# Kernel optimization log

Measured on AMD Instinct MI355X. Metric: run time of the kernel, lower is better.

Reference implementation:

```python
import jax, jax.numpy as jnp
import numpy as np

HEAD_SIZE = 64
N_EMBD = 768

def setup_inputs() -> dict:
    key = jax.random.key(0)
    kx, kq, kk, kv = jax.random.split(key, 4)
    x = jax.random.normal(kx, (4, 4096, N_EMBD), dtype=jnp.float32)
    s = 1.0 / np.sqrt(N_EMBD)
    Wq = jax.random.normal(kq, (N_EMBD, HEAD_SIZE), dtype=jnp.float32) * s
    Wk = jax.random.normal(kk, (N_EMBD, HEAD_SIZE), dtype=jnp.float32) * s
    Wv = jax.random.normal(kv, (N_EMBD, HEAD_SIZE), dtype=jnp.float32) * s
    return {"x": x, "Wq": Wq, "Wk": Wk, "Wv": Wv}

def reference(x, Wq, Wk, Wv):
    b, t, c = x.shape
    h = Wq.shape[1]
    q = jnp.einsum('btc,ch->bth', x, Wq)
    k = jnp.einsum('btc,ch->bth', x, Wk)
    v = jnp.einsum('btc,ch->bth', x, Wv)
    scores = jnp.einsum('bqh,bkh->bqk', q, k) / jnp.sqrt(jnp.float32(h))
    causal = jnp.tril(jnp.ones((t, t), dtype=bool))  # [t,t]
    scores = jnp.where(causal, scores, -jnp.inf)
    attn = jax.nn.softmax(scores, axis=-1)
    return jnp.einsum('bqk,bkh->bqh', attn, v)
```

## Files before the change

kernel.cpp:

```cpp
#include <hip/hip_runtime.h>
#include <math.h>

#define BB 4
#define TT 4096
#define CC 768
#define HH 64
#define NN 192
#define LDP 72
#define GR 32
#define XSTR 776
#define SC2 0.180336880f

typedef __bf16 bf16x8 __attribute__((ext_vector_type(8)));
typedef float floatx4 __attribute__((ext_vector_type(4)));
typedef float floatx16 __attribute__((ext_vector_type(16)));
typedef unsigned short u16x8 __attribute__((ext_vector_type(8)));

__device__ inline unsigned short f2bf(float f) {
    union { __bf16 b; unsigned short u; } v;
    v.b = (__bf16)f;
    return v.u;
}
__device__ inline float bf2f(unsigned short u) {
    union { unsigned int u; float f; } v;
    v.u = (unsigned int)u << 16;
    return v.f;
}
__device__ inline unsigned cvtpk(float lo, float hi) {
    unsigned d;
    asm("v_cvt_pk_bf16_f32 %0, %1, %2" : "=v"(d) : "v"(lo), "v"(hi));
    return d;
}

__global__ __launch_bounds__(256) void wprep(const float* __restrict__ Wq,
                                             const float* __restrict__ Wk,
                                             const float* __restrict__ Wv,
                                             unsigned short* __restrict__ wtf) {
    const int idx = blockIdx.x * 256 + threadIdx.x;
    if (idx >= NN * CC) return;
    const int j = idx & 7;
    const int lane = (idx >> 3) & 63;
    const int rest = idx >> 9;
    const int kg = rest % 24;
    const int n_tile = rest / 24;
    const int c = kg * 32 + (lane >> 4) * 8 + j;
    const int n = n_tile * 16 + (lane & 15);
    const float* W = (n < 64) ? Wq : (n < 128) ? Wk : Wv;
    wtf[idx] = f2bf(W[c * HH + (n & 63)]);
}

__global__ __launch_bounds__(256) void qkv_gemm(const float* __restrict__ x,
                                                const unsigned short* __restrict__ wtf,
                                                unsigned short* __restrict__ qb,
                                                unsigned short* __restrict__ kb,
                                                unsigned short* __restrict__ vbt) {
    __shared__ unsigned short As[GR * XSTR];

    const int tid = threadIdx.x;
    const int w = tid >> 6, lane = tid & 63;
    const int l15 = lane & 15, quad = lane >> 4;
    const int m0 = blockIdx.x * GR;
    const int n0 = w * 48;
    const int nt0 = w * 3;

    const float* xbase = x + (size_t)m0 * CC;
#pragma unroll
    for (int e = 0; e < 12; ++e) {
        const int c = tid + 256 * e;
        const int r = c / 96, off = (c - r * 96) * 8;
        const float4 v0 = *(const float4*)(xbase + (size_t)c * 8);
        const float4 v1 = *(const float4*)(xbase + (size_t)c * 8 + 4);
        u16x8 pk;
        pk[0] = f2bf(v0.x); pk[1] = f2bf(v0.y); pk[2] = f2bf(v0.z); pk[3] = f2bf(v0.w);
        pk[4] = f2bf(v1.x); pk[5] = f2bf(v1.y); pk[6] = f2bf(v1.z); pk[7] = f2bf(v1.w);
        *(u16x8*)(As + r * XSTR + off) = pk;
    }
    __syncthreads();

    floatx4 acc[2][3] = {};
#pragma unroll 4
    for (int step = 0; step < 12; ++step) {
        bf16x8 a0[2], a1[2];
#pragma unroll
        for (int rg = 0; rg < 2; ++rg) {
            const unsigned short* ap = As + (16 * rg + l15) * XSTR + step * 64 + quad * 8;
            a0[rg] = *(const bf16x8*)(ap);
            a1[rg] = *(const bf16x8*)(ap + 32);
        }
#pragma unroll
        for (int j = 0; j < 3; ++j) {
            const unsigned short* bp =
                wtf + ((size_t)((nt0 + j) * 24 + 2 * step) * 64 + lane) * 8;
            const bf16x8 b0 = *(const bf16x8*)(bp);
            const bf16x8 b1 = *(const bf16x8*)(bp + 512);
#pragma unroll
            for (int rg = 0; rg < 2; ++rg) {
                acc[rg][j] = __builtin_amdgcn_mfma_f32_16x16x32_bf16(a0[rg], b0, acc[rg][j], 0, 0, 0);
                acc[rg][j] = __builtin_amdgcn_mfma_f32_16x16x32_bf16(a1[rg], b1, acc[rg][j], 0, 0, 0);
            }
        }
    }

    const int b = m0 >> 12;
#pragma unroll
    for (int j = 0; j < 3; ++j) {
        const int n = n0 + j * 16 + l15;
        const int mid = n >> 6;
        const int h = n & 63;
#pragma unroll
        for (int rg = 0; rg < 2; ++rg) {
            const int tloc = (m0 & (TT - 1)) + 16 * rg + quad * 4;
            if (mid == 2) {
                ushort4 pk;
                pk.x = f2bf(acc[rg][j][0]); pk.y = f2bf(acc[rg][j][1]);
                pk.z = f2bf(acc[rg][j][2]); pk.w = f2bf(acc[rg][j][3]);
                *(ushort4*)(vbt + ((size_t)b * HH + h) * TT + tloc) = pk;
            } else {
                unsigned short* dst = (mid == 0) ? qb : kb;
#pragma unroll
                for (int r = 0; r < 4; ++r)
                    dst[(size_t)(m0 + 16 * rg + quad * 4 + r) * HH + h] = f2bf(acc[rg][j][r]);
            }
        }
    }
}

template<int CH>
__global__ __launch_bounds__(256) void attn_part(const unsigned short* __restrict__ qb,
                                                 const unsigned short* __restrict__ kb,
                                                 const unsigned short* __restrict__ vbt,
                                                 unsigned short* __restrict__ Opart,
                                                 float* __restrict__ lsum,
                                                 float* __restrict__ out) {
    __shared__ __align__(16) unsigned short Ks[64 * 64];
    __shared__ __align__(16) unsigned short VTs[64 * 64];

    constexpr int W  = CH / 2;
    constexpr int NB = 32 / W;
    constexpr int NG = NB;
    constexpr int TOTB = W * NB * (NB + 1) / 2;

    const int b = blockIdx.x & 3;
    int rem = TOTB - 1 - (blockIdx.x >> 2);
    int g = 0;
    while (rem >= W * (g + 1)) { rem -= W * (g + 1); ++g; }
    const int qt = g * W + rem / (g + 1);
    const int ch = rem - (rem / (g + 1)) * (g + 1);

    const int q0  = qt * 128;
    const int tid = threadIdx.x;
    const int w = tid >> 6, lane = tid & 63;
    const int l31 = lane & 31, hi = lane >> 5;
    const int qbase = q0 + 32 * w;

    const unsigned short* Qb  = qb  + (size_t)b * TT * HH;
    const unsigned short* Kb  = kb  + (size_t)b * TT * HH;
    const unsigned short* VTb = vbt + (size_t)b * HH * TT;

    bf16x8 qf[4];
    {
        const unsigned short* qp = Qb + (size_t)(qbase + l31) * HH + 8 * hi;
#pragma unroll
        for (int s = 0; s < 4; ++s) qf[s] = *(const bf16x8*)(qp + 16 * s);
    }

    floatx16 o0 = {}, o1 = {};
    float lacc = 0.f;

    const int nkt = 2 * qt + 2;
    const int kt0 = ch * CH;
    const int kt1 = min(kt0 + CH, nkt);

    const int sr = tid >> 3;
    const int slot = tid & 7;
    const int swz = ((slot ^ (sr & 7)) << 3);

    const int krow_off0 = l31 * 64;
    const int ksw = (l31 & 7);
    const int vd0 = l31, vd1 = 32 + l31;

    u16x8 nk0, nk1, nv0, nv1;
    {
        const unsigned short* Kt = Kb + (size_t)(kt0 * 64) * HH;
        const unsigned short* Vt = VTb + kt0 * 64;
        nk0 = *(const u16x8*)(Kt + (size_t)sr * HH + slot * 8);
        nk1 = *(const u16x8*)(Kt + (size_t)(sr + 32) * HH + slot * 8);
        nv0 = *(const u16x8*)(Vt + (size_t)sr * TT + slot * 8);
        nv1 = *(const u16x8*)(Vt + (size_t)(sr + 32) * TT + slot * 8);
    }

    for (int kt = kt0; kt < kt1; ++kt) {
        __syncthreads();
        *(u16x8*)(Ks  + sr * 64 + swz)        = nk0;
        *(u16x8*)(Ks  + (sr + 32) * 64 + swz) = nk1;
        *(u16x8*)(VTs + sr * 64 + swz)        = nv0;
        *(u16x8*)(VTs + (sr + 32) * 64 + swz) = nv1;
        __syncthreads();

        if (kt + 1 < kt1) {
            const unsigned short* Kt = Kb + (size_t)((kt + 1) * 64) * HH;
            const unsigned short* Vt = VTb + (kt + 1) * 64;
            nk0 = *(const u16x8*)(Kt + (size_t)sr * HH + slot * 8);
            nk1 = *(const u16x8*)(Kt + (size_t)(sr + 32) * HH + slot * 8);
            nv0 = *(const u16x8*)(Vt + (size_t)sr * TT + slot * 8);
            nv1 = *(const u16x8*)(Vt + (size_t)(sr + 32) * TT + slot * 8);
        }

#pragma unroll
        for (int ks = 0; ks < 2; ++ks) {
            const int kb32 = kt * 64 + 32 * ks;
            if (kb32 > qbase + 31) continue;

            bf16x8 kc[4];
#pragma unroll
            for (int s = 0; s < 4; ++s) {
                const int sl = 2 * s + hi;
                kc[s] = *(const bf16x8*)(Ks + 32 * 64 * ks + krow_off0 + ((sl ^ ksw) << 3));
            }

            floatx16 sa = {};
#pragma unroll
            for (int s = 0; s < 4; ++s)
                sa = __builtin_amdgcn_mfma_f32_32x32x16_bf16(kc[s], qf[s], sa, 0, 0, 0);

            float st[16];
#pragma unroll
            for (int r = 0; r < 16; ++r) st[r] = sa[r] * SC2;

            if (kb32 == qbase) {
#pragma unroll
                for (int r = 0; r < 16; ++r) {
                    const int key = (r & 3) + 8 * (r >> 2) + 4 * hi;
                    if (key > l31) st[r] = -INFINITY;
                }
            }

#pragma unroll
            for (int r = 0; r < 16; ++r) {
                const float p = exp2f(st[r]);
                st[r] = p;
                lacc += p;
            }

            bf16x8 pf[2];
#pragma unroll
            for (int m = 0; m < 2; ++m) {
                const unsigned d0 = cvtpk(st[8 * m + 0], st[8 * m + 1]);
                const unsigned d1 = cvtpk(st[8 * m + 2], st[8 * m + 3]);
                const unsigned d2 = cvtpk(st[8 * m + 4], st[8 * m + 5]);
                const unsigned d3 = cvtpk(st[8 * m + 6], st[8 * m + 7]);
                const unsigned e0 = (unsigned)__shfl_xor((int)d0, 32);
                const unsigned e1 = (unsigned)__shfl_xor((int)d1, 32);
                const unsigned e2 = (unsigned)__shfl_xor((int)d2, 32);
                const unsigned e3 = (unsigned)__shfl_xor((int)d3, 32);
                union { unsigned u[4]; bf16x8 v; } pk;
                pk.u[0] = hi ? e2 : d0;
                pk.u[1] = hi ? e3 : d1;
                pk.u[2] = hi ? d2 : e0;
                pk.u[3] = hi ? d3 : e1;
                pf[m] = pk.v;
            }

            bf16x8 vv[4];
#pragma unroll
            for (int i = 0; i < 4; ++i) {
                const int db = i >> 1, m = i & 1;
                const int d = db ? vd1 : vd0;
                const int sl = 4 * ks + 2 * m + hi;
                vv[i] = *(const bf16x8*)(VTs + d * 64 + ((sl ^ (d & 7)) << 3));
            }

            o0 = __builtin_amdgcn_mfma_f32_32x32x16_bf16(vv[0], pf[0], o0, 0, 0, 0);
            o0 = __builtin_amdgcn_mfma_f32_32x32x16_bf16(vv[1], pf[1], o0, 0, 0, 0);
            o1 = __builtin_amdgcn_mfma_f32_32x32x16_bf16(vv[2], pf[0], o1, 0, 0, 0);
            o1 = __builtin_amdgcn_mfma_f32_32x32x16_bf16(vv[3], pf[1], o1, 0, 0, 0);
        }
    }

    const float l = lacc + __shfl_xor(lacc, 32);

    if (qt < W) {
        float* outp = out + ((size_t)b * TT + qbase + l31) * HH;
        const float inv = 1.f / l;
#pragma unroll
        for (int r = 0; r < 16; ++r) {
            const int dd = (r & 3) + 8 * (r >> 2) + 4 * hi;
            outp[dd]      = o0[r] * inv;
            outp[32 + dd] = o1[r] * inv;
        }
        return;
    }

    const int pbase = ((b * 32 + qt) * NG + ch) * 128;
    unsigned short* Op = Opart + ((size_t)pbase + 32 * w + l31) * HH;
#pragma unroll
    for (int a = 0; a < 4; ++a) {
        *(unsigned*)(Op + 8 * a + 4 * hi)          = cvtpk(o0[4 * a + 0], o0[4 * a + 1]);
        *(unsigned*)(Op + 8 * a + 4 * hi + 2)      = cvtpk(o0[4 * a + 2], o0[4 * a + 3]);
        *(unsigned*)(Op + 32 + 8 * a + 4 * hi)     = cvtpk(o1[4 * a + 0], o1[4 * a + 1]);
        *(unsigned*)(Op + 32 + 8 * a + 4 * hi + 2) = cvtpk(o1[4 * a + 2], o1[4 * a + 3]);
    }
    if (hi == 0) lsum[pbase + 32 * w + l31] = l;
}

template<int CH>
__global__ __launch_bounds__(256) void attn_merge(const unsigned short* __restrict__ Opart,
                                                  const float* __restrict__ lsum,
                                                  float* __restrict__ out) {
    constexpr int W  = CH / 2;
    constexpr int NG = 32 / W;
    const int g = blockIdx.x * 256 + threadIdx.x;
    const int row = g >> 3, oct = g & 7;
    const int b = row >> 12, t = row & (TT - 1);
    const int qt = t >> 7, rloc = t & 127;
    if (qt < W) return;
    const int nchunk = qt / W + 1;
    const int pbase = ((b * 32 + qt) * NG) * 128 + rloc;
    const int d0 = oct * 8;

    float L = 0.f;
    float a[8] = {};
    for (int c = 0; c < nchunk; ++c) {
        const int idx = pbase + c * 128;
        L += lsum[idx];
        const u16x8 pv = *(const u16x8*)(Opart + (size_t)idx * HH + d0);
#pragma unroll
        for (int k = 0; k < 8; ++k) a[k] += bf2f(pv[k]);
    }
    const float inv = 1.f / L;
    float4 o0, o1;
    o0.x = a[0] * inv; o0.y = a[1] * inv; o0.z = a[2] * inv; o0.w = a[3] * inv;
    o1.x = a[4] * inv; o1.y = a[5] * inv; o1.z = a[6] * inv; o1.w = a[7] * inv;
    float* dst = out + (size_t)row * HH + d0;
    *(float4*)(dst) = o0;
    *(float4*)(dst + 4) = o1;
}

__global__ __launch_bounds__(256) void attn_full(const unsigned short* __restrict__ qb,
                                                 const unsigned short* __restrict__ kb,
                                                 const unsigned short* __restrict__ vbt,
                                                 float* __restrict__ out) {
    __shared__ unsigned short Ks[64 * LDP];
    __shared__ unsigned short VTs[64 * LDP];
    __shared__ unsigned short Ps[4][16 * LDP];

    const int b   = blockIdx.x >> 6;
    const int qt  = blockIdx.x & 63;
    const int q0  = qt * 64;
    const int tid = threadIdx.x;
    const int w = tid >> 6, lane = tid & 63;
    const int l15 = lane & 15, quad = lane >> 4;

    const unsigned short* Qb  = qb  + (size_t)b * TT * HH;
    const unsigned short* Kb  = kb  + (size_t)b * TT * HH;
    const unsigned short* VTb = vbt + (size_t)b * HH * TT;

    const int qrow = q0 + 16 * w + l15;
    const bf16x8 qf0 = *(const bf16x8*)(Qb + (size_t)qrow * HH + quad * 8);
    const bf16x8 qf1 = *(const bf16x8*)(Qb + (size_t)qrow * HH + 32 + quad * 8);

    floatx4 O[4] = {};
    floatx4 lacc = {0.f, 0.f, 0.f, 0.f};

    for (int kt = 0; kt <= qt; ++kt) {
        __syncthreads();
        const unsigned short* Kt = Kb + (size_t)(kt * 64) * HH;
        const unsigned short* Vt = VTb + kt * 64;
#pragma unroll
        for (int e = 0; e < 2; ++e) {
            const int chunk = tid + 256 * e;
            const int r = chunk >> 3, c0 = (chunk & 7) * 8;
            *(u16x8*)(Ks + r * LDP + c0)  = *(const u16x8*)(Kt + r * HH + c0);
            *(u16x8*)(VTs + r * LDP + c0) = *(const u16x8*)(Vt + (size_t)r * TT + c0);
        }
        __syncthreads();

        floatx4 s[4];
#pragma unroll
        for (int ki = 0; ki < 4; ++ki) {
            const bf16x8 kf0 = *(const bf16x8*)(Ks + (16 * ki + l15) * LDP + quad * 8);
            const bf16x8 kf1 = *(const bf16x8*)(Ks + (16 * ki + l15) * LDP + 32 + quad * 8);
            floatx4 c = {};
            c = __builtin_amdgcn_mfma_f32_16x16x32_bf16(qf0, kf0, c, 0, 0, 0);
            c = __builtin_amdgcn_mfma_f32_16x16x32_bf16(qf1, kf1, c, 0, 0, 0);
            s[ki] = c * SC2;
        }
        if (kt == qt) {
#pragma unroll
            for (int ki = 0; ki < 4; ++ki)
#pragma unroll
                for (int r = 0; r < 4; ++r)
                    if (16 * ki + l15 > 16 * w + quad * 4 + r) s[ki][r] = -INFINITY;
        }
#pragma unroll
        for (int ki = 0; ki < 4; ++ki)
#pragma unroll
            for (int r = 0; r < 4; ++r) {
                const float p = exp2f(s[ki][r]);
                s[ki][r] = p; lacc[r] += p;
            }

        unsigned short* Pw = Ps[w];
#pragma unroll
        for (int ki = 0; ki < 4; ++ki)
#pragma unroll
            for (int r = 0; r < 4; ++r)
                Pw[(quad * 4 + r) * LDP + 16 * ki + l15] = f2bf(s[ki][r]);

        const bf16x8 pf0 = *(const bf16x8*)(Pw + l15 * LDP + quad * 8);
        const bf16x8 pf1 = *(const bf16x8*)(Pw + l15 * LDP + 32 + quad * 8);
#pragma unroll
        for (int di = 0; di < 4; ++di) {
            const bf16x8 vf0 = *(const bf16x8*)(VTs + (16 * di + l15) * LDP + quad * 8);
            const bf16x8 vf1 = *(const bf16x8*)(VTs + (16 * di + l15) * LDP + 32 + quad * 8);
            O[di] = __builtin_amdgcn_mfma_f32_16x16x32_bf16(pf0, vf0, O[di], 0, 0, 0);
            O[di] = __builtin_amdgcn_mfma_f32_16x16x32_bf16(pf1, vf1, O[di], 0, 0, 0);
        }
    }
    float l_r[4];
#pragma unroll
    for (int r = 0; r < 4; ++r) {
        float v = lacc[r];
#pragma unroll
        for (int msk = 8; msk >= 1; msk >>= 1) v += __shfl_xor(v, msk, 64);
        l_r[r] = v;
    }
    float* outp = out + ((size_t)b * TT + q0 + 16 * w) * HH;
#pragma unroll
    for (int di = 0; di < 4; ++di)
#pragma unroll
        for (int r = 0; r < 4; ++r)
            outp[(quad * 4 + r) * HH + 16 * di + l15] = O[di][r] / l_r[r];
}

extern "C" void kernel_launch(void* const* d_in, const int* in_sizes, int n_in,
                              void* d_out, int out_size, void* d_ws, size_t ws_size,
                              hipStream_t stream) {
    const float* x  = (const float*)d_in[0];
    const float* Wq = (const float*)d_in[1];
    const float* Wk = (const float*)d_in[2];
    const float* Wv = (const float*)d_in[3];
    float* out = (float*)d_out;

    const size_t nQKV = (size_t)BB * TT * HH;
    unsigned short* qb  = (unsigned short*)d_ws;
    unsigned short* kb  = qb + nQKV;
    unsigned short* vbt = kb + nQKV;
    unsigned short* wtf = vbt + nQKV;
    unsigned short* Opart = wtf + (size_t)NN * CC;

    const size_t prows8  = (size_t)BB * 32 * 8 * 128;
    const size_t prows16 = (size_t)BB * 32 * 4 * 128;
    float* lsum8  = (float*)(Opart + prows8 * HH);
    float* lsum16 = (float*)(Opart + prows16 * HH);
    const size_t need8  = (size_t)((char*)(lsum8  + prows8)  - (char*)d_ws);
    const size_t need16 = (size_t)((char*)(lsum16 + prows16) - (char*)d_ws);

    wprep<<<(NN * CC + 255) / 256, 256, 0, stream>>>(Wq, Wk, Wv, wtf);
    qkv_gemm<<<(BB * TT) / GR, 256, 0, stream>>>(x, wtf, qb, kb, vbt);
    if (ws_size >= need8) {
        attn_part<8><<<BB * 144, 256, 0, stream>>>(qb, kb, vbt, Opart, lsum8, out);
        attn_merge<8><<<(BB * TT * 8) / 256, 256, 0, stream>>>(Opart, lsum8, out);
    } else if (ws_size >= need16) {
        attn_part<16><<<BB * 80, 256, 0, stream>>>(qb, kb, vbt, Opart, lsum16, out);
        attn_merge<16><<<(BB * TT * 8) / 256, 256, 0, stream>>>(Opart, lsum16, out);
    } else {
        attn_full<<<BB * (TT / 64), 256, 0, stream>>>(qb, kb, vbt, out);
    }
}
```

Baseline: 128.9 us.

## Double-buffer x chunks in QKV GEMM to overlap global loads with MFMA

The QKV projection kernel no longer loads the whole 32x768 x tile into LDS before computing. It now streams four 192-column chunks through a double-buffered LDS area, prefetching the next chunk into registers while MFMAs run on the current one. This is meant to hide global-load latency and shrink LDS use, which could raise occupancy. The cost is an extra barrier per chunk and more live registers for the prefetched data.

```diff
diff --git a/kernel.cpp b/kernel.cpp
--- a/kernel.cpp
+++ b/kernel.cpp
@@ -8,7 +8,8 @@
 #define NN 192
 #define LDP 72
 #define GR 32
-#define XSTR 776
+#define CK 192
+#define ASTR 200
 #define SC2 0.180336880f
 
 typedef __bf16 bf16x8 __attribute__((ext_vector_type(8)));
@@ -54,7 +55,7 @@
                                                 unsigned short* __restrict__ qb,
                                                 unsigned short* __restrict__ kb,
                                                 unsigned short* __restrict__ vbt) {
-    __shared__ unsigned short As[GR * XSTR];
+    __shared__ unsigned short As[2 * GR * ASTR];
 
     const int tid = threadIdx.x;
     const int w = tid >> 6, lane = tid & 63;
@@ -63,43 +64,77 @@
     const int n0 = w * 48;
     const int nt0 = w * 3;
 
-    const float* xbase = x + (size_t)m0 * CC;
-#pragma unroll
-    for (int e = 0; e < 12; ++e) {
-        const int c = tid + 256 * e;
-        const int r = c / 96, off = (c - r * 96) * 8;
-        const float4 v0 = *(const float4*)(xbase + (size_t)c * 8);
-        const float4 v1 = *(const float4*)(xbase + (size_t)c * 8 + 4);
-        u16x8 pk;
-        pk[0] = f2bf(v0.x); pk[1] = f2bf(v0.y); pk[2] = f2bf(v0.z); pk[3] = f2bf(v0.w);
-        pk[4] = f2bf(v1.x); pk[5] = f2bf(v1.y); pk[6] = f2bf(v1.z); pk[7] = f2bf(v1.w);
-        *(u16x8*)(As + r * XSTR + off) = pk;
-    }
-    __syncthreads();
+    int srow[3], sgrp[3];
+#pragma unroll
+    for (int g = 0; g < 3; ++g) {
+        const int flat = tid + 256 * g;
+        srow[g] = flat / 24;
+        sgrp[g] = flat - srow[g] * 24;
+    }
+
+    float4 xr[6];
+#define LOADC(c)                                                               \
+    {                                                                          \
+        _Pragma("unroll")                                                      \
+        for (int g = 0; g < 3; ++g) {                                          \
+            const float* p = x + (size_t)(m0 + srow[g]) * CC + (c) * CK        \
+                             + sgrp[g] * 8;                                    \
+            xr[2 * g]     = *(const float4*)(p);                               \
+            xr[2 * g + 1] = *(const float4*)(p + 4);                           \
+        }                                                                      \
+    }
+#define WRITEC(c)                                                              \
+    {                                                                          \
+        unsigned short* Ab = As + ((c) & 1) * (GR * ASTR);                     \
+        _Pragma("unroll")                                                      \
+        for (int g = 0; g < 3; ++g) {                                          \
+            union { unsigned u[4]; u16x8 v; } pk;                              \
+            pk.u[0] = cvtpk(xr[2 * g].x, xr[2 * g].y);                         \
+            pk.u[1] = cvtpk(xr[2 * g].z, xr[2 * g].w);                         \
+            pk.u[2] = cvtpk(xr[2 * g + 1].x, xr[2 * g + 1].y);                 \
+            pk.u[3] = cvtpk(xr[2 * g + 1].z, xr[2 * g + 1].w);                 \
+            *(u16x8*)(Ab + srow[g] * ASTR + sgrp[g] * 8) = pk.v;               \
+        }                                                                      \
+    }
+
+    LOADC(0);
+    WRITEC(0);
+    LOADC(1);
 
     floatx4 acc[2][3] = {};
-#pragma unroll 4
-    for (int step = 0; step < 12; ++step) {
-        bf16x8 a0[2], a1[2];
-#pragma unroll
-        for (int rg = 0; rg < 2; ++rg) {
-            const unsigned short* ap = As + (16 * rg + l15) * XSTR + step * 64 + quad * 8;
-            a0[rg] = *(const bf16x8*)(ap);
-            a1[rg] = *(const bf16x8*)(ap + 32);
-        }
-#pragma unroll
-        for (int j = 0; j < 3; ++j) {
-            const unsigned short* bp =
-                wtf + ((size_t)((nt0 + j) * 24 + 2 * step) * 64 + lane) * 8;
-            const bf16x8 b0 = *(const bf16x8*)(bp);
-            const bf16x8 b1 = *(const bf16x8*)(bp + 512);
+    for (int c = 0; c < 4; ++c) {
+        const unsigned short* Ab = As + (c & 1) * (GR * ASTR);
+        __syncthreads();
+#pragma unroll
+        for (int s = 0; s < 3; ++s) {
+            bf16x8 a0[2], a1[2];
 #pragma unroll
             for (int rg = 0; rg < 2; ++rg) {
-                acc[rg][j] = __builtin_amdgcn_mfma_f32_16x16x32_bf16(a0[rg], b0, acc[rg][j], 0, 0, 0);
-                acc[rg][j] = __builtin_amdgcn_mfma_f32_16x16x32_bf16(a1[rg], b1, acc[rg][j], 0, 0, 0);
-            }
-        }
-    }
+                const unsigned short* ap = Ab + (16 * rg + l15) * ASTR + s * 64 + quad * 8;
+                a0[rg] = *(const bf16x8*)(ap);
+                a1[rg] = *(const bf16x8*)(ap + 32);
+            }
+            const int gstep = 3 * c + s;
+#pragma unroll
+            for (int j = 0; j < 3; ++j) {
+                const unsigned short* bp =
+                    wtf + ((size_t)((nt0 + j) * 24 + 2 * gstep) * 64 + lane) * 8;
+                const bf16x8 b0 = *(const bf16x8*)(bp);
+                const bf16x8 b1 = *(const bf16x8*)(bp + 512);
+#pragma unroll
+                for (int rg = 0; rg < 2; ++rg) {
+                    acc[rg][j] = __builtin_amdgcn_mfma_f32_16x16x32_bf16(a0[rg], b0, acc[rg][j], 0, 0, 0);
+                    acc[rg][j] = __builtin_amdgcn_mfma_f32_16x16x32_bf16(a1[rg], b1, acc[rg][j], 0, 0, 0);
+                }
+            }
+        }
+        if (c + 1 < 4) {
+            WRITEC(c + 1);
+            if (c + 2 < 4) LOADC(c + 2);
+        }
+    }
+#undef LOADC
+#undef WRITEC
 
     const int b = m0 >> 12;
 #pragma unroll
```

Measured after the change: 127.0 us, median of 2. Within noise of the previous version (-1.5%).
